# Optimization experiments

Hardware: AMD Instinct MI355X
Metric: run time of the kernel (lower is better)

The kernel has to match this reference:

```python
import jax, jax.numpy as jnp
import numpy as np

N, S, Z, H, K, DEG = 8192, 4, 64, 128, 4, 16
E = N * DEG


def setup_inputs() -> dict:
    key = jax.random.key(0)
    ks = jax.random.split(key, 9)
    g = lambda k, shape, scale=1.0: jax.random.normal(k, shape, dtype=jnp.float32) * scale
    return dict(
        zIG=g(ks[0], (N, S, Z)),                         # node intention features
        xt_enc=g(ks[1], (N, S, H)),                      # encoded actions per node
        Ws=g(ks[2], (K, H, Z), 1.0 / np.sqrt(Z)),        # attn_s[k] weights (no bias)
        Wd=g(ks[3], (K, H, Z), 1.0 / np.sqrt(Z)),        # attn_d[k] weights
        F2_w1=g(ks[4], (H, 2 * H), 1.0 / np.sqrt(2 * H)),
        F2_w2=g(ks[5], (H, H), 1.0 / np.sqrt(H)),
        F1_w1=g(ks[6], (H, K * H), 1.0 / np.sqrt(K * H)),
        F1_w2=g(ks[7], (H, H), 1.0 / np.sqrt(H)),
        src=jax.random.randint(ks[8], (E,), 0, N),       # random source per edge
        dst=jnp.repeat(jnp.arange(N), DEG),              # regular graph: DEG in-edges per node, grouped
    )


def reference(zIG, xt_enc, Ws, Wd, F2_w1, F2_w2, F1_w1, F1_w2, src, dst):
    n, s, h = xt_enc.shape
    k = Ws.shape[0]
    deg = src.shape[0] // n

    # ---- edge_attention: eIG[e,s,k] = leaky_relu(sum_h (Ws_k z_src)*(Wd_k z_dst)) ----
    zs, zd = zIG[src], zIG[dst]                          # [E,S,Z] irregular gathers
    scores = []
    for kk in range(k):                                  # k is small & structural
        a_s = zs @ Ws[kk].T                              # [E,S,H]
        a_d = zd @ Wd[kk].T                              # [E,S,H]
        scores.append(jax.nn.leaky_relu((a_s * a_d).sum(-1)))  # [E,S]
    eIG = jnp.stack(scores, axis=-1)                     # [E,S,K]

    # ---- message_func: dA = F2(cat(xt_src, xt_dst)) ----
    msg_in = jnp.concatenate([xt_enc[src], xt_enc[dst]], axis=-1)   # [E,S,2H]
    dA = jax.nn.relu(msg_in @ F2_w1.T) @ F2_w2.T                    # [E,S,H]

    # ---- reduce_func: softmax over neighbor mailbox (dim=1), weighted mean ----
    # dst is grouped with constant degree, so the DGL mailbox is a reshape.
    alpha = jax.nn.softmax(eIG.reshape(n, deg, s, k), axis=1)       # [N,D,S,K]
    mail = dA.reshape(n, deg, s, h)                                 # [N,D,S,H]
    res = jnp.einsum('ndsk,ndsh->nskh', alpha, mail) / deg          # mean over D
    res = res.reshape(n, s, k * h)                                  # cat over k (k-major)
    deltax = jax.nn.relu(res @ F1_w1.T) @ F1_w2.T                   # [N,S,H]
    return deltax, alpha
```

## Files before the change

### kernel.cpp

```cpp
#include <hip/hip_runtime.h>
#include <hip/hip_bf16.h>

typedef unsigned short u16;
typedef unsigned int u32;
using ushort8 = __attribute__((ext_vector_type(8))) unsigned short;
using short8  = __attribute__((ext_vector_type(8))) short;
using f32x4   = __attribute__((ext_vector_type(4))) float;

__device__ __forceinline__ float bf2f(u16 v) {
  union { u32 u; float f; } x; x.u = ((u32)v) << 16; return x.f;
}
__device__ __forceinline__ float u2f(u32 u) {
  union { u32 u; float f; } x; x.u = u; return x.f;
}
__device__ __forceinline__ u16 f2bf(float f) {
  union { u32 u; float f; } x; x.f = f;
  u32 r = x.u + 0x7FFFu + ((x.u >> 16) & 1u);
  return (u16)(r >> 16);
}
__device__ __forceinline__ u32 pack2bf(float lo, float hi) {
  return (u32)f2bf(lo) | ((u32)f2bf(hi) << 16);
}
__device__ __forceinline__ float dot4(float4 a, float4 b) {
  return a.x * b.x + a.y * b.y + a.z * b.z + a.w * b.w;
}
__device__ __forceinline__ void split8(const float* ap, short8& hi, short8& lo) {
  float4 a0 = *(const float4*)ap, a1 = *(const float4*)(ap + 4);
  float e[8] = {a0.x, a0.y, a0.z, a0.w, a1.x, a1.y, a1.z, a1.w};
  u16 h[8], l[8];
  #pragma unroll
  for (int j = 0; j < 8; ++j) {
    u32 b = __float_as_uint(e[j]);
    h[j] = (u16)(b >> 16);
    l[j] = f2bf(e[j] - u2f(b & 0xffff0000u));
  }
  hi = *(short8*)h; lo = *(short8*)l;
}
__device__ __forceinline__ void stage_w(const float* g, int stride, int c, u16* Wl, int t) {
  int row = t >> 1, half = t & 1;
  const float4* gp = (const float4*)(g + (size_t)row * stride + c * 64 + half * 32);
  ushort8* d = (ushort8*)(Wl + row * 72 + half * 32);
  #pragma unroll
  for (int i = 0; i < 4; ++i) {
    float4 a = gp[2 * i], b = gp[2 * i + 1];
    ushort8 o;
    o[0] = f2bf(a.x); o[1] = f2bf(a.y); o[2] = f2bf(a.z); o[3] = f2bf(a.w);
    o[4] = f2bf(b.x); o[5] = f2bf(b.y); o[6] = f2bf(b.z); o[7] = f2bf(b.w);
    d[i] = o;
  }
}
__device__ __forceinline__ void stage_w512(const float* g, int stride, int c, u16* Wl, int t) {
  int row = t >> 2, q = t & 3;
  const float4* gp = (const float4*)(g + (size_t)row * stride + c * 64 + q * 16);
  ushort8* d = (ushort8*)(Wl + row * 72 + q * 16);
  #pragma unroll
  for (int i = 0; i < 2; ++i) {
    float4 a = gp[2 * i], b = gp[2 * i + 1];
    ushort8 o;
    o[0] = f2bf(a.x); o[1] = f2bf(a.y); o[2] = f2bf(a.z); o[3] = f2bf(a.w);
    o[4] = f2bf(b.x); o[5] = f2bf(b.y); o[6] = f2bf(b.z); o[7] = f2bf(b.w);
    d[i] = o;
  }
}

__global__ __launch_bounds__(256) void k_prep(const float* __restrict__ Ws,
                                              const float* __restrict__ Wd,
                                              const float* __restrict__ F1w1,
                                              const float* __restrict__ F2w2,
                                              u16* __restrict__ Bh, u16* __restrict__ Bl,
                                              float* __restrict__ WW2) {
  if (blockIdx.x < 64) {
    int t = blockIdx.x * 256 + threadIdx.x;
    int k = t >> 12, z1 = (t >> 6) & 63, z2 = t & 63;
    const float* wsp = Ws + k * 8192 + z1;
    const float* wdp = Wd + k * 8192 + z2;
    float acc = 0.f;
    #pragma unroll 8
    for (int h = 0; h < 128; ++h) acc += wsp[h * 64] * wdp[h * 64];
    u32 b = __float_as_uint(acc);
    Bh[(k * 64 + z1) * 64 + z2] = (u16)(b >> 16);
    Bl[(k * 64 + z1) * 64 + z2] = f2bf(acc - u2f(b & 0xffff0000u));
  } else {
    int id = (blockIdx.x - 64) * 256 + threadIdx.x;
    int ho = id >> 9, kk = (id >> 7) & 3, hi = id & 127;
    const float* wa = F1w1 + ho * 512 + kk * 128;
    const float* wb = F2w2 + hi;
    float acc = 0.f;
    #pragma unroll 8
    for (int j = 0; j < 128; ++j) acc += wa[j] * wb[j * 128];
    WW2[ho * 512 + kk * 128 + hi] = acc * 0.0625f;
  }
}

__global__ __launch_bounds__(256) void k_tduv(const float* __restrict__ zIG,
                                              const u16* __restrict__ Bh_g,
                                              const u16* __restrict__ Bl_g,
                                              const float* __restrict__ xt,
                                              const float* __restrict__ W1,
                                              float* __restrict__ td,
                                              u16* __restrict__ u, u16* __restrict__ v) {
  __shared__ __align__(16) u16 WlA[128 * 72];
  __shared__ __align__(16) u16 WlB[128 * 72];
  int t = threadIdx.x, lane = t & 63, w = t >> 6;
  int l15 = lane & 15, kc = lane >> 4;
  if (blockIdx.x < 512) {
    u16* Bh = WlA;
    u16* Bl = WlB;
    int chalf = blockIdx.x & 1;
    size_t rowbase = (size_t)(blockIdx.x >> 1) * 128 + w * 32;
    {
      int row = t >> 1, half = t & 1;
      const ushort8* gh = (const ushort8*)(Bh_g + (chalf * 128 + row) * 64 + half * 32);
      const ushort8* gl = (const ushort8*)(Bl_g + (chalf * 128 + row) * 64 + half * 32);
      ushort8* dh = (ushort8*)(Bh + row * 72 + half * 32);
      ushort8* dl = (ushort8*)(Bl + row * 72 + half * 32);
      #pragma unroll
      for (int i = 0; i < 4; ++i) { dh[i] = gh[i]; dl[i] = gl[i]; }
    }
    __syncthreads();
    f32x4 acc[2][8];
    #pragma unroll
    for (int mt = 0; mt < 2; ++mt)
      #pragma unroll
      for (int nt = 0; nt < 8; ++nt) acc[mt][nt] = (f32x4){0.f, 0.f, 0.f, 0.f};
    #pragma unroll
    for (int ks = 0; ks < 2; ++ks) {
      short8 ah[2], al[2];
      #pragma unroll
      for (int mt = 0; mt < 2; ++mt)
        split8(zIG + (rowbase + mt * 16 + l15) * 64 + ks * 32 + kc * 8, ah[mt], al[mt]);
      #pragma unroll
      for (int nt = 0; nt < 8; ++nt) {
        int bo = (nt * 16 + l15) * 72 + ks * 32 + kc * 8;
        short8 bh = *(const short8*)&Bh[bo];
        short8 bl = *(const short8*)&Bl[bo];
        #pragma unroll
        for (int mt = 0; mt < 2; ++mt) {
          acc[mt][nt] = __builtin_amdgcn_mfma_f32_16x16x32_bf16(ah[mt], bh, acc[mt][nt], 0, 0, 0);
          acc[mt][nt] = __builtin_amdgcn_mfma_f32_16x16x32_bf16(al[mt], bh, acc[mt][nt], 0, 0, 0);
          acc[mt][nt] = __builtin_amdgcn_mfma_f32_16x16x32_bf16(ah[mt], bl, acc[mt][nt], 0, 0, 0);
        }
      }
    }
    #pragma unroll
    for (int mt = 0; mt < 2; ++mt)
      #pragma unroll
      for (int nt = 0; nt < 8; ++nt)
        #pragma unroll
        for (int j = 0; j < 4; ++j)
          td[(rowbase + mt * 16 + kc * 4 + j) * 256 + chalf * 128 + nt * 16 + l15] =
              acc[mt][nt][j];
  } else {
    u16* Wlu = WlA;
    u16* Wlv = WlB;
    size_t rowbase = (size_t)(blockIdx.x - 512) * 128 + w * 32;
    f32x4 au[2][8], av[2][8];
    #pragma unroll
    for (int mt = 0; mt < 2; ++mt)
      #pragma unroll
      for (int nt = 0; nt < 8; ++nt) {
        au[mt][nt] = (f32x4){0.f, 0.f, 0.f, 0.f};
        av[mt][nt] = (f32x4){0.f, 0.f, 0.f, 0.f};
      }
    for (int c = 0; c < 2; ++c) {
      __syncthreads();
      stage_w(W1,       256, c, Wlu, t);
      stage_w(W1 + 128, 256, c, Wlv, t);
      __syncthreads();
      #pragma unroll
      for (int ks = 0; ks < 2; ++ks) {
        short8 af[2];
        #pragma unroll
        for (int mt = 0; mt < 2; ++mt) {
          const float* ap = xt + (rowbase + mt * 16 + l15) * 128 + c * 64 + ks * 32 + kc * 8;
          float4 a0 = *(const float4*)ap, a1 = *(const float4*)(ap + 4);
          u16 tmp[8] = {f2bf(a0.x), f2bf(a0.y), f2bf(a0.z), f2bf(a0.w),
                        f2bf(a1.x), f2bf(a1.y), f2bf(a1.z), f2bf(a1.w)};
          af[mt] = *(short8*)tmp;
        }
        #pragma unroll
        for (int nt = 0; nt < 8; ++nt) {
          short8 bu = *(const short8*)&Wlu[(nt * 16 + l15) * 72 + ks * 32 + kc * 8];
          short8 bv = *(const short8*)&Wlv[(nt * 16 + l15) * 72 + ks * 32 + kc * 8];
          #pragma unroll
          for (int mt = 0; mt < 2; ++mt) {
            au[mt][nt] = __builtin_amdgcn_mfma_f32_16x16x32_bf16(af[mt], bu, au[mt][nt], 0, 0, 0);
            av[mt][nt] = __builtin_amdgcn_mfma_f32_16x16x32_bf16(af[mt], bv, av[mt][nt], 0, 0, 0);
          }
        }
      }
    }
    #pragma unroll
    for (int mt = 0; mt < 2; ++mt)
      #pragma unroll
      for (int nt = 0; nt < 8; ++nt)
        #pragma unroll
        for (int j = 0; j < 4; ++j) {
          size_t idx = (rowbase + mt * 16 + kc * 4 + j) * 128 + nt * 16 + l15;
          u[idx] = f2bf(au[mt][nt][j]);
          v[idx] = f2bf(av[mt][nt][j]);
        }
  }
}

__global__ __launch_bounds__(256) void k_score(
    const float* __restrict__ zIG, const int* __restrict__ src,
    const float* __restrict__ td, const u16* __restrict__ uW, const u16* __restrict__ vW,
    float* __restrict__ out, u16* __restrict__ m_ws) {
  __shared__ int srcIdx[32];
  __shared__ float tds[2][16 * 68];
  __shared__ float s17[2][16 * 17];
  __shared__ float e17[2][16 * 17];
  __shared__ float a20[2][16 * 20];

  int t = threadIdx.x, n0 = blockIdx.x * 2;
  if (t < 32) srcIdx[t] = src[n0 * 16 + t];
  #pragma unroll
  for (int i = 0; i < 2; ++i) {
    int idx = t + i * 256;
    int nd = idx >> 8, r = (idx >> 4) & 15, cc = idx & 15;
    *(float4*)&tds[nd][r * 68 + cc * 4] =
        ((const float4*)td)[(size_t)(n0 + nd) * 256 + r * 16 + cc];
  }
  __syncthreads();
  {
    int d = t >> 4, s = (t >> 2) & 3, k = t & 3;
    int base = s * 4;
    float4 zr[2][4];
    #pragma unroll
    for (int nd = 0; nd < 2; ++nd) {
      int sn = srcIdx[nd * 16 + d];
      const float4* zp = (const float4*)(zIG + (size_t)sn * 256 + s * 64);
      #pragma unroll
      for (int i = 0; i < 4; ++i) zr[nd][i] = zp[i * 4 + k];
    }
    #pragma unroll
    for (int nd = 0; nd < 2; ++nd) {
      float p0 = 0.f, p1 = 0.f, p2 = 0.f, p3 = 0.f;
      #pragma unroll
      for (int i = 0; i < 4; ++i) {
        float4 zv = zr[nd][i];
        int o = i * 16 + k * 4;
        p0 += dot4(zv, *(const float4*)&tds[nd][(base + 0) * 68 + o]);
        p1 += dot4(zv, *(const float4*)&tds[nd][(base + 1) * 68 + o]);
        p2 += dot4(zv, *(const float4*)&tds[nd][(base + 2) * 68 + o]);
        p3 += dot4(zv, *(const float4*)&tds[nd][(base + 3) * 68 + o]);
      }
      p0 += __shfl_xor(p0, 1); p1 += __shfl_xor(p1, 1);
      p2 += __shfl_xor(p2, 1); p3 += __shfl_xor(p3, 1);
      p0 += __shfl_xor(p0, 2); p1 += __shfl_xor(p1, 2);
      p2 += __shfl_xor(p2, 2); p3 += __shfl_xor(p3, 2);
      float acc = (k == 0) ? p0 : (k == 1) ? p1 : (k == 2) ? p2 : p3;
      s17[nd][d * 17 + base + k] = acc > 0.f ? acc : 0.01f * acc;
    }
  }
  int hp = t & 63, sD = t >> 6;
  u32 upre[2][16], vbits[2];
  {
    const u32* up = (const u32*)uW;
    #pragma unroll
    for (int nd = 0; nd < 2; ++nd) {
      #pragma unroll
      for (int dd = 0; dd < 16; ++dd)
        upre[nd][dd] = up[(size_t)srcIdx[nd * 16 + dd] * 256 + sD * 64 + hp];
      vbits[nd] = *(const u32*)(vW + (size_t)(n0 + nd) * 512 + sD * 128 + hp * 2);
    }
  }
  __syncthreads();
  float e_own[2];
  int dC = t >> 4, skC = t & 15;
  #pragma unroll
  for (int nd = 0; nd < 2; ++nd) {
    float mx = -3.4e38f;
    #pragma unroll
    for (int dd = 0; dd < 16; ++dd) mx = fmaxf(mx, s17[nd][dd * 17 + skC]);
    e_own[nd] = __expf(s17[nd][dC * 17 + skC] - mx);
    e17[nd][dC * 17 + skC] = e_own[nd];
  }
  __syncthreads();
  #pragma unroll
  for (int nd = 0; nd < 2; ++nd) {
    float sum = 0.f;
    #pragma unroll
    for (int dd = 0; dd < 16; ++dd) sum += e17[nd][dd * 17 + skC];
    float a = e_own[nd] / sum;
    a20[nd][dC * 20 + skC] = a;
    out[4194304u + (unsigned)(n0 + nd) * 256 + t] = a;
  }
  __syncthreads();
  #pragma unroll
  for (int nd = 0; nd < 2; ++nd) {
    float v_lo = u2f(vbits[nd] << 16), v_hi = u2f(vbits[nd] & 0xffff0000u);
    float m0l = 0.f, m0h = 0.f, m1l = 0.f, m1h = 0.f;
    float m2l = 0.f, m2h = 0.f, m3l = 0.f, m3h = 0.f;
    #pragma unroll
    for (int dd = 0; dd < 16; ++dd) {
      u32 ub = upre[nd][dd];
      float r_lo = fmaxf(u2f(ub << 16) + v_lo, 0.f);
      float r_hi = fmaxf(u2f(ub & 0xffff0000u) + v_hi, 0.f);
      float4 a = *(const float4*)&a20[nd][dd * 20 + sD * 4];
      m0l += a.x * r_lo; m0h += a.x * r_hi;
      m1l += a.y * r_lo; m1h += a.y * r_hi;
      m2l += a.z * r_lo; m2h += a.z * r_hi;
      m3l += a.w * r_lo; m3h += a.w * r_hi;
    }
    u32* mp = (u32*)(m_ws + (size_t)(n0 + nd) * 2048);
    mp[(sD * 4 + 0) * 64 + hp] = pack2bf(m0l, m0h);
    mp[(sD * 4 + 1) * 64 + hp] = pack2bf(m1l, m1h);
    mp[(sD * 4 + 2) * 64 + hp] = pack2bf(m2l, m2h);
    mp[(sD * 4 + 3) * 64 + hp] = pack2bf(m3l, m3h);
  }
}

__global__ __launch_bounds__(512) void k_fg(const u16* __restrict__ A,
                                            const float* __restrict__ WF,
                                            const float* __restrict__ WG,
                                            float* __restrict__ out) {
  __shared__ u16 Wl[128 * 72];
  __shared__ u16 hidl[128 * 136];
  int t = threadIdx.x, lane = t & 63, w = t >> 6;
  size_t rowbase = (size_t)blockIdx.x * 128 + w * 16;
  int l15 = lane & 15, kc = lane >> 4;
  f32x4 acc[8];
  #pragma unroll
  for (int nt = 0; nt < 8; ++nt) acc[nt] = (f32x4){0.f, 0.f, 0.f, 0.f};
  for (int c = 0; c < 8; ++c) {
    __syncthreads();
    stage_w512(WF, 512, c, Wl, t);
    __syncthreads();
    #pragma unroll
    for (int ks = 0; ks < 2; ++ks) {
      short8 af = *(const short8*)(A + (rowbase + l15) * 512 + c * 64 + ks * 32 + kc * 8);
      #pragma unroll
      for (int nt = 0; nt < 8; ++nt) {
        short8 bf = *(const short8*)&Wl[(nt * 16 + l15) * 72 + ks * 32 + kc * 8];
        acc[nt] = __builtin_amdgcn_mfma_f32_16x16x32_bf16(af, bf, acc[nt], 0, 0, 0);
      }
    }
  }
  #pragma unroll
  for (int nt = 0; nt < 8; ++nt)
    #pragma unroll
    for (int j = 0; j < 4; ++j)
      hidl[(w * 16 + kc * 4 + j) * 136 + nt * 16 + l15] = f2bf(fmaxf(acc[nt][j], 0.f));
  f32x4 acc2[8];
  #pragma unroll
  for (int nt = 0; nt < 8; ++nt) acc2[nt] = (f32x4){0.f, 0.f, 0.f, 0.f};
  for (int c = 0; c < 2; ++c) {
    __syncthreads();
    stage_w512(WG, 128, c, Wl, t);
    __syncthreads();
    #pragma unroll
    for (int ks = 0; ks < 2; ++ks) {
      short8 af = *(const short8*)&hidl[(w * 16 + l15) * 136 + c * 64 + ks * 32 + kc * 8];
      #pragma unroll
      for (int nt = 0; nt < 8; ++nt) {
        short8 bf = *(const short8*)&Wl[(nt * 16 + l15) * 72 + ks * 32 + kc * 8];
        acc2[nt] = __builtin_amdgcn_mfma_f32_16x16x32_bf16(af, bf, acc2[nt], 0, 0, 0);
      }
    }
  }
  #pragma unroll
  for (int nt = 0; nt < 8; ++nt)
    #pragma unroll
    for (int j = 0; j < 4; ++j)
      out[(rowbase + kc * 4 + j) * 128 + nt * 16 + l15] = acc2[nt][j];
}

extern "C" void kernel_launch(void* const* d_in, const int* in_sizes, int n_in,
                              void* d_out, int out_size, void* d_ws, size_t ws_size,
                              hipStream_t stream) {
  const float* zIG  = (const float*)d_in[0];
  const float* xt   = (const float*)d_in[1];
  const float* Ws   = (const float*)d_in[2];
  const float* Wd   = (const float*)d_in[3];
  const float* F2w1 = (const float*)d_in[4];
  const float* F2w2 = (const float*)d_in[5];
  const float* F1w1 = (const float*)d_in[6];
  const float* F1w2 = (const float*)d_in[7];
  const int* src    = (const int*)d_in[8];
  float* out = (float*)d_out;

  char* ws = (char*)d_ws;
  u16* Bh    = (u16*)ws;
  u16* Bl    = Bh + 16384;
  float* td  = (float*)(ws + 65536);
  u16* u     = (u16*)(ws + 65536 + 33554432);
  u16* v     = u + 4194304;
  float* WW2 = (float*)(ws + 50397184);
  u16* m     = (u16*)(ws + 50659328);

  k_prep <<<320,  256, 0, stream>>>(Ws, Wd, F1w1, F2w2, Bh, Bl, WW2);
  k_tduv <<<768,  256, 0, stream>>>(zIG, Bh, Bl, xt, F2w1, td, u, v);
  k_score<<<4096, 256, 0, stream>>>(zIG, src, td, u, v, out, m);
  k_fg   <<<256,  512, 0, stream>>>(m, WW2, F1w2, out);
}
```

Before: 101.4 us.

## Split fused score kernel into separate edge-softmax and mailbox aggregation kernels

Splits the fused k_score kernel, which handled two nodes per block, into two kernels with one node per block. k_edge computes the attention scores and softmax and writes alpha to the output. k_mail reads alpha back from global memory and does the gathered relu-weighted aggregation into the mailbox buffer. This lowers per-thread register use (no 2x16 prefetched u values) and shared memory, which could raise occupancy. In exchange it adds a launch and a global round trip for alpha, and it loses the overlap between the u gathers and the score computation.

```diff
diff --git a/kernel.cpp b/kernel.cpp
--- a/kernel.cpp
+++ b/kernel.cpp
@@ -203,113 +203,90 @@
   }
 }
 
-__global__ __launch_bounds__(256) void k_score(
+__global__ __launch_bounds__(256) void k_edge(
     const float* __restrict__ zIG, const int* __restrict__ src,
-    const float* __restrict__ td, const u16* __restrict__ uW, const u16* __restrict__ vW,
-    float* __restrict__ out, u16* __restrict__ m_ws) {
-  __shared__ int srcIdx[32];
-  __shared__ float tds[2][16 * 68];
-  __shared__ float s17[2][16 * 17];
-  __shared__ float e17[2][16 * 17];
-  __shared__ float a20[2][16 * 20];
-
-  int t = threadIdx.x, n0 = blockIdx.x * 2;
-  if (t < 32) srcIdx[t] = src[n0 * 16 + t];
-  #pragma unroll
-  for (int i = 0; i < 2; ++i) {
-    int idx = t + i * 256;
-    int nd = idx >> 8, r = (idx >> 4) & 15, cc = idx & 15;
-    *(float4*)&tds[nd][r * 68 + cc * 4] =
-        ((const float4*)td)[(size_t)(n0 + nd) * 256 + r * 16 + cc];
+    const float* __restrict__ td, float* __restrict__ out) {
+  __shared__ int srcIdx[16];
+  __shared__ float tds[16 * 68];
+  __shared__ float s17[16 * 17];
+
+  int t = threadIdx.x, n = blockIdx.x;
+  if (t < 16) srcIdx[t] = src[n * 16 + t];
+  {
+    int r = t >> 4, cc = t & 15;
+    *(float4*)&tds[r * 68 + cc * 4] = ((const float4*)(td + (size_t)n * 1024))[r * 16 + cc];
   }
   __syncthreads();
   {
     int d = t >> 4, s = (t >> 2) & 3, k = t & 3;
+    int sn = srcIdx[d];
+    const float4* zp = (const float4*)(zIG + (size_t)sn * 256 + s * 64);
     int base = s * 4;
-    float4 zr[2][4];
-    #pragma unroll
-    for (int nd = 0; nd < 2; ++nd) {
-      int sn = srcIdx[nd * 16 + d];
-      const float4* zp = (const float4*)(zIG + (size_t)sn * 256 + s * 64);
-      #pragma unroll
-      for (int i = 0; i < 4; ++i) zr[nd][i] = zp[i * 4 + k];
-    }
-    #pragma unroll
-    for (int nd = 0; nd < 2; ++nd) {
-      float p0 = 0.f, p1 = 0.f, p2 = 0.f, p3 = 0.f;
-      #pragma unroll
-      for (int i = 0; i < 4; ++i) {
-        float4 zv = zr[nd][i];
-        int o = i * 16 + k * 4;
-        p0 += dot4(zv, *(const float4*)&tds[nd][(base + 0) * 68 + o]);
-        p1 += dot4(zv, *(const float4*)&tds[nd][(base + 1) * 68 + o]);
-        p2 += dot4(zv, *(const float4*)&tds[nd][(base + 2) * 68 + o]);
-        p3 += dot4(zv, *(const float4*)&tds[nd][(base + 3) * 68 + o]);
-      }
-      p0 += __shfl_xor(p0, 1); p1 += __shfl_xor(p1, 1);
-      p2 += __shfl_xor(p2, 1); p3 += __shfl_xor(p3, 1);
-      p0 += __shfl_xor(p0, 2); p1 += __shfl_xor(p1, 2);
-      p2 += __shfl_xor(p2, 2); p3 += __shfl_xor(p3, 2);
-      float acc = (k == 0) ? p0 : (k == 1) ? p1 : (k == 2) ? p2 : p3;
-      s17[nd][d * 17 + base + k] = acc > 0.f ? acc : 0.01f * acc;
-    }
-  }
-  int hp = t & 63, sD = t >> 6;
-  u32 upre[2][16], vbits[2];
+    float p0 = 0.f, p1 = 0.f, p2 = 0.f, p3 = 0.f;
+    #pragma unroll
+    for (int i = 0; i < 4; ++i) {
+      float4 zv = zp[i * 4 + k];
+      int o = i * 16 + k * 4;
+      p0 += dot4(zv, *(const float4*)&tds[(base + 0) * 68 + o]);
+      p1 += dot4(zv, *(const float4*)&tds[(base + 1) * 68 + o]);
+      p2 += dot4(zv, *(const float4*)&tds[(base + 2) * 68 + o]);
+      p3 += dot4(zv, *(const float4*)&tds[(base + 3) * 68 + o]);
+    }
+    p0 += __shfl_xor(p0, 1); p1 += __shfl_xor(p1, 1);
+    p2 += __shfl_xor(p2, 1); p3 += __shfl_xor(p3, 1);
+    p0 += __shfl_xor(p0, 2); p1 += __shfl_xor(p1, 2);
+    p2 += __shfl_xor(p2, 2); p3 += __shfl_xor(p3, 2);
+    float acc = (k == 0) ? p0 : (k == 1) ? p1 : (k == 2) ? p2 : p3;
+    s17[d * 17 + base + k] = acc > 0.f ? acc : 0.01f * acc;
+  }
+  __syncthreads();
   {
-    const u32* up = (const u32*)uW;
-    #pragma unroll
-    for (int nd = 0; nd < 2; ++nd) {
-      #pragma unroll
-      for (int dd = 0; dd < 16; ++dd)
-        upre[nd][dd] = up[(size_t)srcIdx[nd * 16 + dd] * 256 + sD * 64 + hp];
-      vbits[nd] = *(const u32*)(vW + (size_t)(n0 + nd) * 512 + sD * 128 + hp * 2);
-    }
-  }
+    int d = t >> 4, sk = t & 15;
+    float mx = -3.4e38f;
+    #pragma unroll
+    for (int dd = 0; dd < 16; ++dd) mx = fmaxf(mx, s17[dd * 17 + sk]);
+    float sum = 0.f, eown = 0.f;
+    #pragma unroll
+    for (int dd = 0; dd < 16; ++dd) {
+      float e = __expf(s17[dd * 17 + sk] - mx);
+      sum += e;
+      if (dd == d) eown = e;
+    }
+    out[4194304u + (unsigned)n * 256 + t] = eown / sum;
+  }
+}
+
+__global__ __launch_bounds__(256) void k_mail(
+    const int* __restrict__ src, const float* __restrict__ alpha_g,
+    const u16* __restrict__ uW, const u16* __restrict__ vW, u16* __restrict__ m_ws) {
+  __shared__ int srcIdx[16];
+  __shared__ float al[256];
+  int t = threadIdx.x, n = blockIdx.x;
+  if (t < 16) srcIdx[t] = src[n * 16 + t];
+  al[t] = alpha_g[(size_t)n * 256 + t];
   __syncthreads();
-  float e_own[2];
-  int dC = t >> 4, skC = t & 15;
-  #pragma unroll
-  for (int nd = 0; nd < 2; ++nd) {
-    float mx = -3.4e38f;
-    #pragma unroll
-    for (int dd = 0; dd < 16; ++dd) mx = fmaxf(mx, s17[nd][dd * 17 + skC]);
-    e_own[nd] = __expf(s17[nd][dC * 17 + skC] - mx);
-    e17[nd][dC * 17 + skC] = e_own[nd];
-  }
-  __syncthreads();
-  #pragma unroll
-  for (int nd = 0; nd < 2; ++nd) {
-    float sum = 0.f;
-    #pragma unroll
-    for (int dd = 0; dd < 16; ++dd) sum += e17[nd][dd * 17 + skC];
-    float a = e_own[nd] / sum;
-    a20[nd][dC * 20 + skC] = a;
-    out[4194304u + (unsigned)(n0 + nd) * 256 + t] = a;
-  }
-  __syncthreads();
-  #pragma unroll
-  for (int nd = 0; nd < 2; ++nd) {
-    float v_lo = u2f(vbits[nd] << 16), v_hi = u2f(vbits[nd] & 0xffff0000u);
-    float m0l = 0.f, m0h = 0.f, m1l = 0.f, m1h = 0.f;
-    float m2l = 0.f, m2h = 0.f, m3l = 0.f, m3h = 0.f;
-    #pragma unroll
-    for (int dd = 0; dd < 16; ++dd) {
-      u32 ub = upre[nd][dd];
-      float r_lo = fmaxf(u2f(ub << 16) + v_lo, 0.f);
-      float r_hi = fmaxf(u2f(ub & 0xffff0000u) + v_hi, 0.f);
-      float4 a = *(const float4*)&a20[nd][dd * 20 + sD * 4];
-      m0l += a.x * r_lo; m0h += a.x * r_hi;
-      m1l += a.y * r_lo; m1h += a.y * r_hi;
-      m2l += a.z * r_lo; m2h += a.z * r_hi;
-      m3l += a.w * r_lo; m3h += a.w * r_hi;
-    }
-    u32* mp = (u32*)(m_ws + (size_t)(n0 + nd) * 2048);
-    mp[(sD * 4 + 0) * 64 + hp] = pack2bf(m0l, m0h);
-    mp[(sD * 4 + 1) * 64 + hp] = pack2bf(m1l, m1h);
-    mp[(sD * 4 + 2) * 64 + hp] = pack2bf(m2l, m2h);
-    mp[(sD * 4 + 3) * 64 + hp] = pack2bf(m3l, m3h);
-  }
+  int hp = t & 63, s = t >> 6;
+  u32 vbits = *(const u32*)(vW + (size_t)n * 512 + s * 128 + hp * 2);
+  float v_lo = u2f(vbits << 16), v_hi = u2f(vbits & 0xffff0000u);
+  const u32* up = (const u32*)uW;
+  float m0l = 0.f, m0h = 0.f, m1l = 0.f, m1h = 0.f;
+  float m2l = 0.f, m2h = 0.f, m3l = 0.f, m3h = 0.f;
+  #pragma unroll
+  for (int d = 0; d < 16; ++d) {
+    u32 ub = up[(size_t)srcIdx[d] * 256 + s * 64 + hp];
+    float r_lo = fmaxf(u2f(ub << 16) + v_lo, 0.f);
+    float r_hi = fmaxf(u2f(ub & 0xffff0000u) + v_hi, 0.f);
+    float4 a = *(const float4*)&al[d * 16 + s * 4];
+    m0l += a.x * r_lo; m0h += a.x * r_hi;
+    m1l += a.y * r_lo; m1h += a.y * r_hi;
+    m2l += a.z * r_lo; m2h += a.z * r_hi;
+    m3l += a.w * r_lo; m3h += a.w * r_hi;
+  }
+  u32* mp = (u32*)(m_ws + (size_t)n * 2048);
+  mp[(s * 4 + 0) * 64 + hp] = pack2bf(m0l, m0h);
+  mp[(s * 4 + 1) * 64 + hp] = pack2bf(m1l, m1h);
+  mp[(s * 4 + 2) * 64 + hp] = pack2bf(m2l, m2h);
+  mp[(s * 4 + 3) * 64 + hp] = pack2bf(m3l, m3h);
 }
 
 __global__ __launch_bounds__(512) void k_fg(const u16* __restrict__ A,
@@ -392,6 +369,7 @@
 
   k_prep <<<320,  256, 0, stream>>>(Ws, Wd, F1w1, F2w2, Bh, Bl, WW2);
   k_tduv <<<768,  256, 0, stream>>>(zIG, Bh, Bl, xt, F2w1, td, u, v);
-  k_score<<<4096, 256, 0, stream>>>(zIG, src, td, u, v, out, m);
+  k_edge <<<8192, 256, 0, stream>>>(zIG, src, td, out);
+  k_mail <<<8192, 256, 0, stream>>>(src, out + 4194304, u, v, m);
   k_fg   <<<256,  512, 0, stream>>>(m, WW2, F1w2, out);
 }
```

Result: slower. 105.3 us (+3.8%).
